# Kernel tuning notes

Hardware: AMD Instinct MI355X
Metric: run time of the kernel (lower is better)

## Reference

```python
import jax, jax.numpy as jnp
import numpy as np


def setup_inputs() -> dict:
    key = jax.random.key(0)
    ks = jax.random.split(key, 8)
    B, C, H, W = 4, 256, 64, 64
    C8 = C // 8
    s = 0.05
    return {
        "x": jax.random.normal(ks[0], (B, C, H, W), jnp.float32),
        "wq": jax.random.normal(ks[1], (C8, C), jnp.float32) * s,
        "bq": jax.random.normal(ks[2], (C8,), jnp.float32) * s,
        "wk": jax.random.normal(ks[3], (C8, C), jnp.float32) * s,
        "bk": jax.random.normal(ks[4], (C8,), jnp.float32) * s,
        "wv": jax.random.normal(ks[5], (C, C), jnp.float32) * s,
        "bv": jax.random.normal(ks[6], (C,), jnp.float32) * s,
        "gamma": jax.random.uniform(ks[7], (1,), jnp.float32),
    }


def reference(x, wq, bq, wk, bk, wv, bv, gamma):
    B, C, H, W = x.shape
    N = H * W
    xf = x.reshape(B, C, N)  # flatten spatial: [B, C, N]
    # 1x1 convs are channel-wise matmuls
    q = jnp.einsum("dc,bcn->bnd", wq, xf) + bq[None, None, :]  # [B, N, C/8]
    k = jnp.einsum("dc,bcn->bdn", wk, xf) + bk[None, :, None]  # [B, C/8, N]
    v = jnp.einsum("dc,bcn->bdn", wv, xf) + bv[None, :, None]  # [B, C, N]
    energy = jnp.einsum("bnd,bdm->bnm", q, k)  # [B, N, N]
    attention = jax.nn.softmax(energy, axis=-1)
    # out = value @ attention^T  -> [B, C, N]
    out = jnp.einsum("bcm,bnm->bcn", v, attention)
    out = out.reshape(B, C, H, W)
    return gamma[0] * out + x
```

## Files before the change

### kernel.cpp

```cpp
#include <hip/hip_runtime.h>
#include <hip/hip_bf16.h>
#include <stdint.h>

#define B_ 4
#define C_ 256
#define N_ 4096
#define D_ 32
#define KT 256

typedef __bf16 bf16_t;
typedef __bf16 bf16x4_t __attribute__((ext_vector_type(4)));
typedef __bf16 bf16x8_t __attribute__((ext_vector_type(8)));
typedef float  f32x4    __attribute__((ext_vector_type(4)));

__global__ __launch_bounds__(256) void cast_w_kernel(
    const float* __restrict__ wq, const float* __restrict__ wk,
    const float* __restrict__ wv, bf16_t* __restrict__ Wb)
{
  const int gr = blockIdx.x;
  const int t  = threadIdx.x;
  float v;
  if (gr < 32)      v = wq[gr * C_ + t];
  else if (gr < 64) v = wk[(gr - 32) * C_ + t];
  else              v = wv[(gr - 64) * C_ + t];
  Wb[gr * C_ + t] = (bf16_t)v;
}

__global__ __launch_bounds__(256) void proj_kernel(
    const float* __restrict__ x, const bf16_t* __restrict__ Wb,
    const float* __restrict__ bq, const float* __restrict__ bk,
    const float* __restrict__ bv,
    bf16_t* __restrict__ Qh, bf16_t* __restrict__ Kh, bf16_t* __restrict__ Vh)
{
  __shared__ float xs[64][65];
  const int bi = blockIdx.x;
  const int b  = bi & 3;
  const int n0 = (bi >> 2) * 64;
  const int t = threadIdx.x, w = t >> 6, lane = t & 63;
  const int l4 = lane >> 4, lm = lane & 15;

  const f32x4 z4 = {0.f, 0.f, 0.f, 0.f};
  f32x4 acc[5][4];
#pragma unroll
  for (int rt = 0; rt < 5; ++rt)
#pragma unroll
    for (int ct = 0; ct < 4; ++ct) acc[rt][ct] = z4;

  const int lr = t >> 2;
  const int lc = (t & 3) * 16;

#pragma unroll 1
  for (int k0 = 0; k0 < C_; k0 += 64) {
    __syncthreads();
#pragma unroll
    for (int i = 0; i < 4; ++i) {
      const f32x4 v = *(const f32x4*)(x + ((size_t)(b * C_ + k0 + lr)) * N_ + n0 + lc + i * 4);
      xs[lr][lc + i * 4 + 0] = v[0];
      xs[lr][lc + i * 4 + 1] = v[1];
      xs[lr][lc + i * 4 + 2] = v[2];
      xs[lr][lc + i * 4 + 3] = v[3];
    }
    __syncthreads();

    bf16x8_t af[5][2], bfr[4][2];
#pragma unroll
    for (int rt = 0; rt < 5; ++rt)
#pragma unroll
      for (int kc = 0; kc < 2; ++kc)
        af[rt][kc] = *(const bf16x8_t*)(Wb + (size_t)(w * 80 + rt * 16 + lm) * C_ + k0 + kc * 32 + l4 * 8);
#pragma unroll
    for (int ct = 0; ct < 4; ++ct)
#pragma unroll
      for (int kc = 0; kc < 2; ++kc) {
        bf16_t tmp[8];
#pragma unroll
        for (int j = 0; j < 8; ++j)
          tmp[j] = (bf16_t)xs[kc * 32 + l4 * 8 + j][ct * 16 + lm];
        bfr[ct][kc] = *(bf16x8_t*)tmp;
      }
#pragma unroll
    for (int rt = 0; rt < 5; ++rt)
#pragma unroll
      for (int ct = 0; ct < 4; ++ct)
#pragma unroll
        for (int kc = 0; kc < 2; ++kc)
          acc[rt][ct] = __builtin_amdgcn_mfma_f32_16x16x32_bf16(af[rt][kc], bfr[ct][kc], acc[rt][ct], 0, 0, 0);
  }

#pragma unroll
  for (int rt = 0; rt < 5; ++rt)
#pragma unroll
    for (int r = 0; r < 4; ++r) {
      const int gr = w * 80 + rt * 16 + 4 * l4 + r;
      const float bias = (gr < 32) ? bq[gr] : (gr < 64) ? bk[gr - 32] : bv[gr - 64];
#pragma unroll
      for (int ct = 0; ct < 4; ++ct) {
        const int n = n0 + ct * 16 + lm;
        float v = acc[rt][ct][r] + bias;
        if (gr < 32) {
          v *= 1.44269504088896f;
          Qh[((size_t)(b * N_ + n)) * D_ + gr] = (bf16_t)v;
        } else if (gr < 64) {
          Kh[((size_t)(b * N_ + n)) * D_ + (gr - 32)] = (bf16_t)v;
        } else {
          Vh[((size_t)(b * C_ + (gr - 64))) * N_ + n] = (bf16_t)v;
        }
      }
    }
}

__global__ __launch_bounds__(1024) void attn_kernel(
    const bf16_t* __restrict__ Qh, const bf16_t* __restrict__ Kh,
    const bf16_t* __restrict__ Vh, const float* __restrict__ x,
    const float* __restrict__ gamma, float* __restrict__ out)
{
  __shared__ __align__(16) bf16_t Pl[2][64][KT];
  __shared__ __align__(16) float  Lx[64][20];

  const int bi = blockIdx.x;
  const int xcd = bi & 7, slot = bi >> 3;
  const int b  = xcd >> 1;
  const int q0 = ((xcd & 1) * 32 + slot) * 64;

  const int t = threadIdx.x, w = t >> 6, lane = t & 63;
  const int l4 = lane >> 4, lm = lane & 15;
  const int cg = w >> 1, kh = w & 1;
  const int swz = (lm & 7) << 3;

  const f32x4 z4 = {0.f, 0.f, 0.f, 0.f};

  bf16x8_t qf[4];
#pragma unroll
  for (int rt = 0; rt < 4; ++rt)
    qf[rt] = *(const bf16x8_t*)(Qh + ((size_t)(b * N_ + q0 + rt * 16 + lm)) * D_ + l4 * 8);

  const bf16_t* kbase = Kh + ((size_t)(b * N_ + w * 16 + lm)) * D_ + l4 * 8;
  const bf16_t* vbase = Vh + ((size_t)(b * C_ + cg * 32 + lm)) * N_ + kh * 128 + l4 * 8;

  f32x4 acc[2][4];
#pragma unroll
  for (int ct = 0; ct < 2; ++ct)
#pragma unroll
    for (int rt = 0; rt < 4; ++rt) acc[ct][rt] = z4;
  float l_run[4] = {0.f, 0.f, 0.f, 0.f};

  bf16x8_t kf;
  kf = *(const bf16x8_t*)(kbase);
  bf16x8_t vf0[2], vf1[2];
#pragma unroll
  for (int ct = 0; ct < 2; ++ct) {
    vf0[ct] = *(const bf16x8_t*)(vbase + (size_t)(ct * 16) * N_);
    vf1[ct] = *(const bf16x8_t*)(vbase + (size_t)(ct * 16) * N_ + 32);
  }

#pragma unroll 1
  for (int it = 0; it < N_ / KT; ++it) {
    const int buf = it & 1;

    f32x4 S[4];
#pragma unroll
    for (int rt = 0; rt < 4; ++rt)
      S[rt] = __builtin_amdgcn_mfma_f32_16x16x32_bf16(kf, qf[rt], z4, 0, 0, 0);

    const int k0n = ((it + 1) * KT) & (N_ - 1);
    bf16x8_t kn = *(const bf16x8_t*)(kbase + (size_t)k0n * D_);

#pragma unroll
    for (int rt = 0; rt < 4; ++rt) {
      const int prow = rt * 16 + lm;
      const float p0 = __builtin_amdgcn_exp2f(S[rt][0]);
      const float p1 = __builtin_amdgcn_exp2f(S[rt][1]);
      const float p2 = __builtin_amdgcn_exp2f(S[rt][2]);
      const float p3 = __builtin_amdgcn_exp2f(S[rt][3]);
      l_run[rt] += (p0 + p1) + (p2 + p3);
      bf16x4_t w4 = {(bf16_t)p0, (bf16_t)p1, (bf16_t)p2, (bf16_t)p3};
      *(bf16x4_t*)&Pl[buf][prow][(w * 16 + 4 * l4) ^ swz] = w4;
    }

    asm volatile("s_waitcnt lgkmcnt(0)" ::: "memory");
    __builtin_amdgcn_s_barrier();

#pragma unroll
    for (int s4 = 0; s4 < 4; ++s4) {
      bf16x8_t pa[4];
#pragma unroll
      for (int rt = 0; rt < 4; ++rt)
        pa[rt] = *(const bf16x8_t*)&Pl[buf][rt * 16 + lm][(kh * 128 + s4 * 32 + l4 * 8) ^ swz];
      const int knx = (it * KT + (s4 + 2) * 32) & 127;
      const int kbase_nx = ((it + (s4 >= 2)) * KT) & (N_ - 1);
      if ((s4 & 1) == 0) {
#pragma unroll
        for (int ct = 0; ct < 2; ++ct)
#pragma unroll
          for (int rt = 0; rt < 4; ++rt)
            acc[ct][rt] = __builtin_amdgcn_mfma_f32_16x16x32_bf16(vf0[ct], pa[rt], acc[ct][rt], 0, 0, 0);
#pragma unroll
        for (int ct = 0; ct < 2; ++ct)
          vf0[ct] = *(const bf16x8_t*)(vbase + (size_t)(ct * 16) * N_ + kbase_nx + knx);
      } else {
#pragma unroll
        for (int ct = 0; ct < 2; ++ct)
#pragma unroll
          for (int rt = 0; rt < 4; ++rt)
            acc[ct][rt] = __builtin_amdgcn_mfma_f32_16x16x32_bf16(vf1[ct], pa[rt], acc[ct][rt], 0, 0, 0);
#pragma unroll
        for (int ct = 0; ct < 2; ++ct)
          vf1[ct] = *(const bf16x8_t*)(vbase + (size_t)(ct * 16) * N_ + kbase_nx + knx);
      }
    }

    kf = kn;
  }

#pragma unroll
  for (int rt = 0; rt < 4; ++rt) {
    l_run[rt] += __shfl_xor(l_run[rt], 16);
    l_run[rt] += __shfl_xor(l_run[rt], 32);
  }
  if (l4 == 0) {
#pragma unroll
    for (int rt = 0; rt < 4; ++rt) Lx[rt * 16 + lm][w] = l_run[rt];
  }

  float* Ax = (float*)&Pl[0][0][0];
  asm volatile("s_waitcnt lgkmcnt(0)" ::: "memory");
  __builtin_amdgcn_s_barrier();

  if (kh == 1) {
#pragma unroll
    for (int rt = 0; rt < 4; ++rt)
#pragma unroll
      for (int ct = 0; ct < 2; ++ct)
        *(f32x4*)&Ax[((cg * 64) + rt * 16 + lm) * 32 + ct * 16 + 4 * l4] = acc[ct][rt];
  }
  asm volatile("s_waitcnt lgkmcnt(0)" ::: "memory");
  __builtin_amdgcn_s_barrier();

  if (kh == 0) {
    const float g = gamma[0];
#pragma unroll
    for (int rt = 0; rt < 4; ++rt) {
      const f32x4 s0 = *(const f32x4*)&Lx[rt * 16 + lm][0];
      const f32x4 s1 = *(const f32x4*)&Lx[rt * 16 + lm][4];
      const f32x4 s2 = *(const f32x4*)&Lx[rt * 16 + lm][8];
      const f32x4 s3 = *(const f32x4*)&Lx[rt * 16 + lm][12];
      const float lt = (((s0[0] + s0[1]) + (s0[2] + s0[3])) + ((s1[0] + s1[1]) + (s1[2] + s1[3]))) +
                       (((s2[0] + s2[1]) + (s2[2] + s2[3])) + ((s3[0] + s3[1]) + (s3[2] + s3[3])));
      const float inv = 1.f / lt;
      const int n = q0 + rt * 16 + lm;
#pragma unroll
      for (int ct = 0; ct < 2; ++ct) {
        const f32x4 other = *(const f32x4*)&Ax[((cg * 64) + rt * 16 + lm) * 32 + ct * 16 + 4 * l4];
#pragma unroll
        for (int r = 0; r < 4; ++r) {
          const int c = cg * 32 + ct * 16 + 4 * l4 + r;
          const size_t idx = ((size_t)(b * C_ + c)) * N_ + n;
          out[idx] = g * ((acc[ct][rt][r] + other[r]) * inv) + x[idx];
        }
      }
    }
  }
}

extern "C" void kernel_launch(void* const* d_in, const int* in_sizes, int n_in,
                              void* d_out, int out_size, void* d_ws, size_t ws_size,
                              hipStream_t stream) {
  const float* x     = (const float*)d_in[0];
  const float* wq    = (const float*)d_in[1];
  const float* bq    = (const float*)d_in[2];
  const float* wk    = (const float*)d_in[3];
  const float* bk    = (const float*)d_in[4];
  const float* wv    = (const float*)d_in[5];
  const float* bv    = (const float*)d_in[6];
  const float* gamma = (const float*)d_in[7];
  float* out = (float*)d_out;

  bf16_t* Qh = (bf16_t*)d_ws;
  bf16_t* Kh = Qh + (size_t)B_ * N_ * D_;
  bf16_t* Vh = Kh + (size_t)B_ * N_ * D_;
  bf16_t* Wb = Vh + (size_t)B_ * C_ * N_;

  cast_w_kernel<<<320, 256, 0, stream>>>(wq, wk, wv, Wb);
  proj_kernel<<<256, 256, 0, stream>>>(x, Wb, bq, bk, bv, Qh, Kh, Vh);
  attn_kernel<<<256, 1024, 0, stream>>>(Qh, Kh, Vh, x, gamma, out);
}
```

Before: 96.36 us.

## Keep softmax probabilities in registers, split keys across waves, drop LDS P staging

The attention kernel now runs 512 threads, with each wave owning a quarter of the key range and half the channels. K rows are permuted so the S MFMA output layout lines up directly as the B operand of the PV MFMA. This removes the per-tile LDS write/read of P and the per-iteration barrier. The cost is a larger accumulator footprint per wave (8x4 tiles) and an LDS-based reduction of partial outputs across the four key-split waves in the epilogue, done in two passes to fit shared memory.

New measurement: 161.8 us. 67.9% more time.

```diff
diff --git a/kernel.cpp b/kernel.cpp
--- a/kernel.cpp
+++ b/kernel.cpp
@@ -6,10 +6,8 @@
 #define C_ 256
 #define N_ 4096
 #define D_ 32
-#define KT 256
 
 typedef __bf16 bf16_t;
-typedef __bf16 bf16x4_t __attribute__((ext_vector_type(4)));
 typedef __bf16 bf16x8_t __attribute__((ext_vector_type(8)));
 typedef float  f32x4    __attribute__((ext_vector_type(4)));
 
@@ -109,13 +107,13 @@
     }
 }
 
-__global__ __launch_bounds__(1024) void attn_kernel(
+__global__ __launch_bounds__(512, 2) void attn_kernel(
     const bf16_t* __restrict__ Qh, const bf16_t* __restrict__ Kh,
     const bf16_t* __restrict__ Vh, const float* __restrict__ x,
     const float* __restrict__ gamma, float* __restrict__ out)
 {
-  __shared__ __align__(16) bf16_t Pl[2][64][KT];
-  __shared__ __align__(16) float  Lx[64][20];
+  __shared__ float Ax[4][256][2][16];
+  __shared__ float Lx[64][8];
 
   const int bi = blockIdx.x;
   const int xcd = bi & 7, slot = bi >> 3;
@@ -124,8 +122,7 @@
 
   const int t = threadIdx.x, w = t >> 6, lane = t & 63;
   const int l4 = lane >> 4, lm = lane & 15;
-  const int cg = w >> 1, kh = w & 1;
-  const int swz = (lm & 7) << 3;
+  const int ks = w & 3, cp = w >> 2;
 
   const f32x4 z4 = {0.f, 0.f, 0.f, 0.f};
 
@@ -134,82 +131,64 @@
   for (int rt = 0; rt < 4; ++rt)
     qf[rt] = *(const bf16x8_t*)(Qh + ((size_t)(b * N_ + q0 + rt * 16 + lm)) * D_ + l4 * 8);
 
-  const bf16_t* kbase = Kh + ((size_t)(b * N_ + w * 16 + lm)) * D_ + l4 * 8;
-  const bf16_t* vbase = Vh + ((size_t)(b * C_ + cg * 32 + lm)) * N_ + kh * 128 + l4 * 8;
-
-  f32x4 acc[2][4];
-#pragma unroll
-  for (int ct = 0; ct < 2; ++ct)
+  const int kperm = 8 * (lm >> 2) + (lm & 3);
+  const bf16_t* kbaseP = Kh + ((size_t)(b * N_ + ks * 64 + kperm)) * D_ + l4 * 8;
+  const bf16_t* vbase = Vh + ((size_t)(b * C_ + cp * 128 + lm)) * N_ + ks * 64 + 8 * l4;
+
+  f32x4 acc[8][4];
+#pragma unroll
+  for (int ct = 0; ct < 8; ++ct)
 #pragma unroll
     for (int rt = 0; rt < 4; ++rt) acc[ct][rt] = z4;
   float l_run[4] = {0.f, 0.f, 0.f, 0.f};
 
-  bf16x8_t kf;
-  kf = *(const bf16x8_t*)(kbase);
-  bf16x8_t vf0[2], vf1[2];
-#pragma unroll
-  for (int ct = 0; ct < 2; ++ct) {
-    vf0[ct] = *(const bf16x8_t*)(vbase + (size_t)(ct * 16) * N_);
-    vf1[ct] = *(const bf16x8_t*)(vbase + (size_t)(ct * 16) * N_ + 32);
-  }
+  bf16x8_t kf[2], kfn[2];
+#pragma unroll
+  for (int mt = 0; mt < 2; ++mt)
+    kf[mt] = *(const bf16x8_t*)(kbaseP + (size_t)(4 * mt) * D_);
 
 #pragma unroll 1
-  for (int it = 0; it < N_ / KT; ++it) {
-    const int buf = it & 1;
-
-    f32x4 S[4];
-#pragma unroll
-    for (int rt = 0; rt < 4; ++rt)
-      S[rt] = __builtin_amdgcn_mfma_f32_16x16x32_bf16(kf, qf[rt], z4, 0, 0, 0);
-
-    const int k0n = ((it + 1) * KT) & (N_ - 1);
-    bf16x8_t kn = *(const bf16x8_t*)(kbase + (size_t)k0n * D_);
-
-#pragma unroll
-    for (int rt = 0; rt < 4; ++rt) {
-      const int prow = rt * 16 + lm;
-      const float p0 = __builtin_amdgcn_exp2f(S[rt][0]);
-      const float p1 = __builtin_amdgcn_exp2f(S[rt][1]);
-      const float p2 = __builtin_amdgcn_exp2f(S[rt][2]);
-      const float p3 = __builtin_amdgcn_exp2f(S[rt][3]);
-      l_run[rt] += (p0 + p1) + (p2 + p3);
-      bf16x4_t w4 = {(bf16_t)p0, (bf16_t)p1, (bf16_t)p2, (bf16_t)p3};
-      *(bf16x4_t*)&Pl[buf][prow][(w * 16 + 4 * l4) ^ swz] = w4;
-    }
-
-    asm volatile("s_waitcnt lgkmcnt(0)" ::: "memory");
-    __builtin_amdgcn_s_barrier();
-
-#pragma unroll
-    for (int s4 = 0; s4 < 4; ++s4) {
-      bf16x8_t pa[4];
-#pragma unroll
-      for (int rt = 0; rt < 4; ++rt)
-        pa[rt] = *(const bf16x8_t*)&Pl[buf][rt * 16 + lm][(kh * 128 + s4 * 32 + l4 * 8) ^ swz];
-      const int knx = (it * KT + (s4 + 2) * 32) & 127;
-      const int kbase_nx = ((it + (s4 >= 2)) * KT) & (N_ - 1);
-      if ((s4 & 1) == 0) {
-#pragma unroll
-        for (int ct = 0; ct < 2; ++ct)
-#pragma unroll
-          for (int rt = 0; rt < 4; ++rt)
-            acc[ct][rt] = __builtin_amdgcn_mfma_f32_16x16x32_bf16(vf0[ct], pa[rt], acc[ct][rt], 0, 0, 0);
-#pragma unroll
-        for (int ct = 0; ct < 2; ++ct)
-          vf0[ct] = *(const bf16x8_t*)(vbase + (size_t)(ct * 16) * N_ + kbase_nx + knx);
-      } else {
-#pragma unroll
-        for (int ct = 0; ct < 2; ++ct)
-#pragma unroll
-          for (int rt = 0; rt < 4; ++rt)
-            acc[ct][rt] = __builtin_amdgcn_mfma_f32_16x16x32_bf16(vf1[ct], pa[rt], acc[ct][rt], 0, 0, 0);
-#pragma unroll
-        for (int ct = 0; ct < 2; ++ct)
-          vf1[ct] = *(const bf16x8_t*)(vbase + (size_t)(ct * 16) * N_ + kbase_nx + knx);
-      }
-    }
-
-    kf = kn;
+  for (int it = 0; it < N_ / 256; ++it) {
+#pragma unroll
+    for (int kg = 0; kg < 2; ++kg) {
+      const int ko = it * 256 + kg * 32;
+
+      bf16x8_t vf[8];
+#pragma unroll
+      for (int ct = 0; ct < 8; ++ct)
+        vf[ct] = *(const bf16x8_t*)(vbase + (size_t)(ct * 16) * N_ + ko);
+
+      const int kon = (kg == 0) ? (ko + 32) : ((ko + 224) & (N_ - 1));
+#pragma unroll
+      for (int mt = 0; mt < 2; ++mt)
+        kfn[mt] = *(const bf16x8_t*)(kbaseP + (size_t)(kon + 4 * mt) * D_);
+
+      bf16x8_t pb[4];
+#pragma unroll
+      for (int rt = 0; rt < 4; ++rt) {
+        const f32x4 S0 = __builtin_amdgcn_mfma_f32_16x16x32_bf16(kf[0], qf[rt], z4, 0, 0, 0);
+        const f32x4 S1 = __builtin_amdgcn_mfma_f32_16x16x32_bf16(kf[1], qf[rt], z4, 0, 0, 0);
+        float p[8];
+#pragma unroll
+        for (int r = 0; r < 4; ++r) p[r]     = __builtin_amdgcn_exp2f(S0[r]);
+#pragma unroll
+        for (int r = 0; r < 4; ++r) p[4 + r] = __builtin_amdgcn_exp2f(S1[r]);
+        l_run[rt] += ((p[0] + p[1]) + (p[2] + p[3])) + ((p[4] + p[5]) + (p[6] + p[7]));
+        bf16_t tmp[8];
+#pragma unroll
+        for (int j = 0; j < 8; ++j) tmp[j] = (bf16_t)p[j];
+        pb[rt] = *(bf16x8_t*)tmp;
+      }
+
+#pragma unroll
+      for (int ct = 0; ct < 8; ++ct)
+#pragma unroll
+        for (int rt = 0; rt < 4; ++rt)
+          acc[ct][rt] = __builtin_amdgcn_mfma_f32_16x16x32_bf16(vf[ct], pb[rt], acc[ct][rt], 0, 0, 0);
+
+      kf[0] = kfn[0];
+      kf[1] = kfn[1];
+    }
   }
 
 #pragma unroll
@@ -222,41 +201,36 @@
     for (int rt = 0; rt < 4; ++rt) Lx[rt * 16 + lm][w] = l_run[rt];
   }
 
-  float* Ax = (float*)&Pl[0][0][0];
-  asm volatile("s_waitcnt lgkmcnt(0)" ::: "memory");
-  __builtin_amdgcn_s_barrier();
-
-  if (kh == 1) {
-#pragma unroll
-    for (int rt = 0; rt < 4; ++rt)
-#pragma unroll
-      for (int ct = 0; ct < 2; ++ct)
-        *(f32x4*)&Ax[((cg * 64) + rt * 16 + lm) * 32 + ct * 16 + 4 * l4] = acc[ct][rt];
-  }
-  asm volatile("s_waitcnt lgkmcnt(0)" ::: "memory");
-  __builtin_amdgcn_s_barrier();
-
-  if (kh == 0) {
-    const float g = gamma[0];
-#pragma unroll
-    for (int rt = 0; rt < 4; ++rt) {
-      const f32x4 s0 = *(const f32x4*)&Lx[rt * 16 + lm][0];
-      const f32x4 s1 = *(const f32x4*)&Lx[rt * 16 + lm][4];
-      const f32x4 s2 = *(const f32x4*)&Lx[rt * 16 + lm][8];
-      const f32x4 s3 = *(const f32x4*)&Lx[rt * 16 + lm][12];
-      const float lt = (((s0[0] + s0[1]) + (s0[2] + s0[3])) + ((s1[0] + s1[1]) + (s1[2] + s1[3]))) +
-                       (((s2[0] + s2[1]) + (s2[2] + s2[3])) + ((s3[0] + s3[1]) + (s3[2] + s3[3])));
+  const float g = gamma[0];
+#pragma unroll 1
+  for (int p = 0; p < 2; ++p) {
+    asm volatile("s_waitcnt lgkmcnt(0)" ::: "memory");
+    __builtin_amdgcn_s_barrier();
+
+#pragma unroll
+    for (int ct = 0; ct < 8; ++ct)
+#pragma unroll
+      for (int rtl = 0; rtl < 2; ++rtl)
+#pragma unroll
+        for (int r = 0; r < 4; ++r)
+          Ax[ks][cp * 128 + ct * 16 + 4 * l4 + r][rtl][lm] = acc[ct][2 * p + rtl][r];
+
+    asm volatile("s_waitcnt lgkmcnt(0)" ::: "memory");
+    __builtin_amdgcn_s_barrier();
+
+#pragma unroll
+    for (int rtl = 0; rtl < 2; ++rtl) {
+      const int ql = 32 * p + rtl * 16 + lm;
+      const float lt = ((Lx[ql][0] + Lx[ql][1]) + (Lx[ql][2] + Lx[ql][3]));
       const float inv = 1.f / lt;
-      const int n = q0 + rt * 16 + lm;
-#pragma unroll
-      for (int ct = 0; ct < 2; ++ct) {
-        const f32x4 other = *(const f32x4*)&Ax[((cg * 64) + rt * 16 + lm) * 32 + ct * 16 + 4 * l4];
-#pragma unroll
-        for (int r = 0; r < 4; ++r) {
-          const int c = cg * 32 + ct * 16 + 4 * l4 + r;
-          const size_t idx = ((size_t)(b * C_ + c)) * N_ + n;
-          out[idx] = g * ((acc[ct][rt][r] + other[r]) * inv) + x[idx];
-        }
+      const int n = q0 + ql;
+#pragma unroll
+      for (int c8 = 0; c8 < 8; ++c8) {
+        const int ch = w * 32 + l4 * 8 + c8;
+        const float s = (Ax[0][ch][rtl][lm] + Ax[1][ch][rtl][lm]) +
+                        (Ax[2][ch][rtl][lm] + Ax[3][ch][rtl][lm]);
+        const size_t idx = ((size_t)(b * C_ + ch)) * N_ + n;
+        out[idx] = g * (s * inv) + x[idx];
       }
     }
   }
@@ -282,5 +256,5 @@
 
   cast_w_kernel<<<320, 256, 0, stream>>>(wq, wk, wv, Wb);
   proj_kernel<<<256, 256, 0, stream>>>(x, Wb, bq, bk, bv, Qh, Kh, Vh);
-  attn_kernel<<<256, 1024, 0, stream>>>(Qh, Kh, Vh, x, gamma, out);
-}
+  attn_kernel<<<256, 512, 0, stream>>>(Qh, Kh, Vh, x, gamma, out);
+}
```
